# Kernel optimization log

Hardware: AMD Instinct MI355X
Metric: run time of the kernel (lower is better)

## Reference

```python
import jax, jax.numpy as jnp
import numpy as np

N = 100000   # nodes
E = 1600000  # edges (avg degree 16)
D = 128      # embedding / hidden dim
L = 2        # aggregator layers (len(weight_size_list)-1)
EPS = 1e-12  # F.normalize eps


def setup_inputs() -> dict:
    key = jax.random.key(0)
    ks = jax.random.split(key, 8)
    return {
        "embeddings": jax.random.normal(ks[0], (N, D), jnp.float32),
        "edge_src": jax.random.randint(ks[1], (E,), 0, N, jnp.int32),
        "edge_dst": jax.random.randint(ks[2], (E,), 0, N, jnp.int32),
        "edge_val": jax.random.uniform(ks[3], (E,), jnp.float32),
        "W_sum": jax.random.normal(ks[4], (L, D, D), jnp.float32) * 0.05,
        "b_sum": jnp.zeros((L, D), jnp.float32),
        "W_prod": jax.random.normal(ks[5], (L, D, D), jnp.float32) * 0.05,
        "b_prod": jnp.zeros((L, D), jnp.float32),
    }


def reference(embeddings, edge_src, edge_dst, edge_val, W_sum, b_sum, W_prod, b_prod):
    # Faithful KGATConv forward with BiAggregator (alg_type='bi'), dropout=0 (eval).
    # Note: original code feeds the UN-normalized aggregator output as `embeddings`
    # (ego) to the next layer, while the SpMM consumes the normalized all_embeddings[-1].
    ego = embeddings            # `embeddings` variable in torch code
    spmm_in = embeddings        # all_embeddings[-1]
    outs = [embeddings]
    for i in range(L):
        # sparse A @ x : gather source rows, scale by edge value, scatter-add to dst
        msg = edge_val[:, None] * spmm_in[edge_src]            # [E, D]
        side = jax.ops.segment_sum(msg, edge_dst, num_segments=N)  # [N, D]
        # BiAggregator: LeakyReLU(W1(e+side)+b1) + LeakyReLU(W2(e*side)+b2)
        s = jax.nn.leaky_relu((ego + side) @ W_sum[i] + b_sum[i], 0.01)
        p = jax.nn.leaky_relu((ego * side) @ W_prod[i] + b_prod[i], 0.01)
        ego = s + p
        # F.normalize(p=2, dim=-1)
        nrm = jnp.maximum(jnp.linalg.norm(ego, axis=-1, keepdims=True), EPS)
        spmm_in = ego / nrm
        outs.append(spmm_in)
    return jnp.stack(outs)  # [L+1, N, D]
```

## Files before the change

kernel.cpp:

```cpp
#include <hip/hip_runtime.h>

#define D_DIM 128
#define ROWS 32
#define MROWS 64
#define ZPAD 136
#define EPAD 132

#define BSH 7
#define BROWS (1 << BSH)
#define NB_MAX 2048
#define CHUNK 4096

typedef __bf16 bf16x8 __attribute__((ext_vector_type(8)));
typedef __bf16 bf16x4 __attribute__((ext_vector_type(4)));
typedef float  f32x4  __attribute__((ext_vector_type(4)));

__global__ __launch_bounds__(256) void spmm_atomic(
    const float* __restrict__ x, const int* __restrict__ src,
    const int* __restrict__ dst, const float* __restrict__ val,
    float* __restrict__ side, long long total)
{
    long long i = (long long)blockIdx.x * blockDim.x + threadIdx.x;
    if (i >= total) return;
    int e = (int)(i >> 5);
    int q = (int)(i & 31);
    int s = src[e];
    int d = dst[e];
    float v = val[e];
    const float4 xv = *reinterpret_cast<const float4*>(x + (long long)s * D_DIM + q * 4);
    float* o = side + (long long)d * D_DIM + q * 4;
    unsafeAtomicAdd(o + 0, v * xv.x);
    unsafeAtomicAdd(o + 1, v * xv.y);
    unsafeAtomicAdd(o + 2, v * xv.z);
    unsafeAtomicAdd(o + 3, v * xv.w);
}

__global__ __launch_bounds__(256) void hist_kernel(
    const int* __restrict__ dst, int* __restrict__ cnt, int E)
{
    int i = blockIdx.x * 256 + threadIdx.x;
    if (i < E) atomicAdd(&cnt[dst[i]], 1);
}

__global__ __launch_bounds__(256) void scan_blocks(
    const int* __restrict__ cnt, int* __restrict__ row_ptr,
    int* __restrict__ blk_sums, int N)
{
    __shared__ int sh[256];
    int i = blockIdx.x * 256 + threadIdx.x;
    int v = (i < N) ? cnt[i] : 0;
    sh[threadIdx.x] = v;
    __syncthreads();
#pragma unroll
    for (int off = 1; off < 256; off <<= 1) {
        int t = (threadIdx.x >= off) ? sh[threadIdx.x - off] : 0;
        __syncthreads();
        sh[threadIdx.x] += t;
        __syncthreads();
    }
    if (i < N) row_ptr[i] = sh[threadIdx.x] - v;
    if (threadIdx.x == 255) blk_sums[blockIdx.x] = sh[255];
}

__global__ __launch_bounds__(256) void scan_carry(int* __restrict__ blk, int B)
{
    __shared__ int sh[256];
    __shared__ int carry;
    if (threadIdx.x == 0) carry = 0;
    __syncthreads();
    for (int base = 0; base < B; base += 256) {
        int i = base + threadIdx.x;
        int v = (i < B) ? blk[i] : 0;
        sh[threadIdx.x] = v;
        __syncthreads();
#pragma unroll
        for (int off = 1; off < 256; off <<= 1) {
            int t = (threadIdx.x >= off) ? sh[threadIdx.x - off] : 0;
            __syncthreads();
            sh[threadIdx.x] += t;
            __syncthreads();
        }
        int excl = sh[threadIdx.x] - v + carry;
        if (i < B) blk[i] = excl;
        __syncthreads();
        if (threadIdx.x == 255) carry = carry + sh[255];
        __syncthreads();
    }
}

__global__ __launch_bounds__(256) void scan_add(
    int* __restrict__ row_ptr, const int* __restrict__ blk_sums,
    int* __restrict__ row_fill, int N, int E)
{
    int i = blockIdx.x * 256 + threadIdx.x;
    if (i < N) {
        int v = row_ptr[i] + blk_sums[i >> 8];
        row_ptr[i]  = v;
        row_fill[i] = v;
    }
    if (i == 0) row_ptr[N] = E;
}

__global__ __launch_bounds__(256) void scatter_kernel(
    const int* __restrict__ src, const int* __restrict__ dst,
    const float* __restrict__ val, int* __restrict__ row_fill,
    int2* __restrict__ csr_sv, int E)
{
    int e = blockIdx.x * 256 + threadIdx.x;
    if (e >= E) return;
    int d = dst[e];
    int pos = atomicAdd(&row_fill[d], 1);
    csr_sv[pos] = make_int2(src[e], __float_as_int(val[e]));
}

__global__ __launch_bounds__(256) void bucket_count(
    const int* __restrict__ dst, int* __restrict__ bucket_cnt, int E, int NB)
{
    __shared__ int h[NB_MAX];
    for (int i = threadIdx.x; i < NB; i += 256) h[i] = 0;
    __syncthreads();
    int ebase = blockIdx.x * CHUNK;
    int ecnt  = min(CHUNK, E - ebase);
    for (int i = threadIdx.x; i < ecnt; i += 256)
        atomicAdd(&h[dst[ebase + i] >> BSH], 1);
    __syncthreads();
    for (int i = threadIdx.x; i < NB; i += 256)
        if (h[i]) atomicAdd(&bucket_cnt[i], h[i]);
}

__global__ __launch_bounds__(256) void bucket_scan(
    const int* __restrict__ bucket_cnt, int* __restrict__ bucket_ptr,
    int* __restrict__ bucket_fill, int NB, int E)
{
    __shared__ int sh[256];
    __shared__ int carry;
    if (threadIdx.x == 0) carry = 0;
    __syncthreads();
    for (int base = 0; base < NB; base += 256) {
        int i = base + threadIdx.x;
        int v = (i < NB) ? bucket_cnt[i] : 0;
        sh[threadIdx.x] = v;
        __syncthreads();
#pragma unroll
        for (int off = 1; off < 256; off <<= 1) {
            int t = (threadIdx.x >= off) ? sh[threadIdx.x - off] : 0;
            __syncthreads();
            sh[threadIdx.x] += t;
            __syncthreads();
        }
        if (i < NB) {
            int excl = sh[threadIdx.x] - v + carry;
            bucket_ptr[i]  = excl;
            bucket_fill[i] = excl;
        }
        __syncthreads();
        if (threadIdx.x == 255) carry = carry + sh[255];
        __syncthreads();
    }
    if (threadIdx.x == 0) bucket_ptr[NB] = E;
}

__global__ __launch_bounds__(256) void bucket_scatter(
    const int* __restrict__ src, const int* __restrict__ dst,
    const float* __restrict__ val, int* __restrict__ bucket_fill,
    int* __restrict__ stage,
    int NB, int E)
{
    __shared__ int hist[NB_MAX];
    __shared__ int excl[NB_MAX];
    __shared__ int gbase[NB_MAX];
    __shared__ int psum[256];
    __shared__ int s_src[CHUNK];
    __shared__ int s_val[CHUNK];
    __shared__ int s_dst[CHUNK];

    const int tid   = threadIdx.x;
    const int ebase = blockIdx.x * CHUNK;
    const int ecnt  = min(CHUNK, E - ebase);

    for (int i = tid; i < NB; i += 256) hist[i] = 0;
    __syncthreads();
    for (int i = tid; i < ecnt; i += 256)
        atomicAdd(&hist[dst[ebase + i] >> BSH], 1);
    __syncthreads();
    const int per = (NB + 255) / 256;
    const int t0  = tid * per;
    int tsum = 0;
    for (int k = 0; k < per; ++k) {
        int idx = t0 + k;
        tsum += (idx < NB) ? hist[idx] : 0;
    }
    psum[tid] = tsum;
    __syncthreads();
#pragma unroll
    for (int off = 1; off < 256; off <<= 1) {
        int t = (tid >= off) ? psum[tid - off] : 0;
        __syncthreads();
        psum[tid] += t;
        __syncthreads();
    }
    int run = psum[tid] - tsum;
    for (int k = 0; k < per; ++k) {
        int idx = t0 + k;
        if (idx < NB) { excl[idx] = run; run += hist[idx]; }
    }
    __syncthreads();
    for (int i = tid; i < NB; i += 256)
        gbase[i] = hist[i] ? atomicAdd(&bucket_fill[i], hist[i]) : 0;
    __syncthreads();
    for (int i = tid; i < NB; i += 256) hist[i] = excl[i];
    __syncthreads();
    for (int i = tid; i < ecnt; i += 256) {
        int d = dst[ebase + i];
        int slot = atomicAdd(&hist[d >> BSH], 1);
        s_src[slot] = src[ebase + i];
        s_val[slot] = __float_as_int(val[ebase + i]);
        s_dst[slot] = d;
    }
    __syncthreads();
    for (int i = tid; i < ecnt; i += 256) {
        int d   = s_dst[i];
        int bkt = d >> BSH;
        int gpos = gbase[bkt] + (i - excl[bkt]);
        *reinterpret_cast<int4*>(stage + 4 * (long long)gpos) =
            make_int4(s_src[i], s_val[i], d, 0);
    }
}

__global__ __launch_bounds__(256) void bucket_finalize(
    const int* __restrict__ stage, const int* __restrict__ bucket_ptr,
    int* __restrict__ row_ptr, int2* __restrict__ csr_sv, int N, int E)
{
    __shared__ int cnt[BROWS];
    __shared__ int rbase[BROWS];

    const int b   = blockIdx.x;
    const int tid = threadIdx.x;
    const int e0  = bucket_ptr[b];
    const int e1  = bucket_ptr[b + 1];
    const int r0  = b << BSH;
    const int nrows = min(BROWS, N - r0);

    if (tid < BROWS) cnt[tid] = 0;
    __syncthreads();
    for (int i = e0 + tid; i < e1; i += 256)
        atomicAdd(&cnt[stage[4 * (long long)i + 2] & (BROWS - 1)], 1);
    __syncthreads();
    if (tid < BROWS) rbase[tid] = cnt[tid];
    __syncthreads();
#pragma unroll
    for (int off = 1; off < BROWS; off <<= 1) {
        int t = 0;
        if (tid < BROWS && tid >= off) t = rbase[tid - off];
        __syncthreads();
        if (tid < BROWS) rbase[tid] += t;
        __syncthreads();
    }
    if (tid < BROWS) {
        int excl = e0 + rbase[tid] - cnt[tid];
        rbase[tid] = excl;
        if (tid < nrows) row_ptr[r0 + tid] = excl;
    }
    if (b == 0 && tid == 0) row_ptr[N] = E;
    __syncthreads();
    if (tid < BROWS) cnt[tid] = 0;
    __syncthreads();
    for (int i = e0 + tid; i < e1; i += 256) {
        const int4 t = *reinterpret_cast<const int4*>(stage + 4 * (long long)i);
        int r = t.z & (BROWS - 1);
        int rank = atomicAdd(&cnt[r], 1);
        csr_sv[rbase[r] + rank] = make_int2(t.x, t.y);
    }
}

__global__ __launch_bounds__(256) void wt_convert(
    const float* __restrict__ Wsum, const float* __restrict__ Wprod,
    __bf16* __restrict__ WTsum, __bf16* __restrict__ WTprod, int total)
{
    int i = blockIdx.x * 256 + threadIdx.x;
    if (i >= total) return;
    int l  = i >> 14;
    int nk = i & 16383;
    int n  = nk >> 7;
    int k  = nk & 127;
    int widx = (l << 14) + (k << 7) + n;
    WTsum[i]  = (__bf16)Wsum[widx];
    WTprod[i] = (__bf16)Wprod[widx];
}

__global__ __launch_bounds__(256) void emb_prep(
    const float* __restrict__ emb, float* __restrict__ out0,
    __bf16* __restrict__ xbf, long long n4)
{
    long long i = (long long)blockIdx.x * 256 + threadIdx.x;
    if (i >= n4) return;
    float4 v = reinterpret_cast<const float4*>(emb)[i];
    reinterpret_cast<float4*>(out0)[i] = v;
    bf16x4 b;
    b[0] = (__bf16)v.x; b[1] = (__bf16)v.y;
    b[2] = (__bf16)v.z; b[3] = (__bf16)v.w;
    reinterpret_cast<bf16x4*>(xbf)[i] = b;
}

__global__ __launch_bounds__(256) void spmm_csr_bf16(
    const __bf16* __restrict__ x, const int* __restrict__ row_ptr,
    const int2* __restrict__ csr_sv, float* __restrict__ side, int N)
{
    int row  = blockIdx.x * 8 + (threadIdx.x >> 5);
    int lane = threadIdx.x & 31;
    if (row >= N) return;
    int start = row_ptr[row];
    int end   = row_ptr[row + 1];
    const __bf16* xl = x + lane * 4;
    float4 acc = make_float4(0.f, 0.f, 0.f, 0.f);
    int j = start;
    for (; j + 8 <= end; j += 8) {
        int2 sv0 = csr_sv[j + 0], sv1 = csr_sv[j + 1];
        int2 sv2 = csr_sv[j + 2], sv3 = csr_sv[j + 3];
        int2 sv4 = csr_sv[j + 4], sv5 = csr_sv[j + 5];
        int2 sv6 = csr_sv[j + 6], sv7 = csr_sv[j + 7];
        bf16x4 b0 = *reinterpret_cast<const bf16x4*>(xl + (long long)sv0.x * D_DIM);
        bf16x4 b1 = *reinterpret_cast<const bf16x4*>(xl + (long long)sv1.x * D_DIM);
        bf16x4 b2 = *reinterpret_cast<const bf16x4*>(xl + (long long)sv2.x * D_DIM);
        bf16x4 b3 = *reinterpret_cast<const bf16x4*>(xl + (long long)sv3.x * D_DIM);
        bf16x4 b4 = *reinterpret_cast<const bf16x4*>(xl + (long long)sv4.x * D_DIM);
        bf16x4 b5 = *reinterpret_cast<const bf16x4*>(xl + (long long)sv5.x * D_DIM);
        bf16x4 b6 = *reinterpret_cast<const bf16x4*>(xl + (long long)sv6.x * D_DIM);
        bf16x4 b7 = *reinterpret_cast<const bf16x4*>(xl + (long long)sv7.x * D_DIM);
        float v0 = __int_as_float(sv0.y), v1 = __int_as_float(sv1.y);
        float v2 = __int_as_float(sv2.y), v3 = __int_as_float(sv3.y);
        float v4 = __int_as_float(sv4.y), v5 = __int_as_float(sv5.y);
        float v6 = __int_as_float(sv6.y), v7 = __int_as_float(sv7.y);
        acc.x += v0 * (float)b0[0] + v1 * (float)b1[0] + v2 * (float)b2[0] + v3 * (float)b3[0];
        acc.y += v0 * (float)b0[1] + v1 * (float)b1[1] + v2 * (float)b2[1] + v3 * (float)b3[1];
        acc.z += v0 * (float)b0[2] + v1 * (float)b1[2] + v2 * (float)b2[2] + v3 * (float)b3[2];
        acc.w += v0 * (float)b0[3] + v1 * (float)b1[3] + v2 * (float)b2[3] + v3 * (float)b3[3];
        acc.x += v4 * (float)b4[0] + v5 * (float)b5[0] + v6 * (float)b6[0] + v7 * (float)b7[0];
        acc.y += v4 * (float)b4[1] + v5 * (float)b5[1] + v6 * (float)b6[1] + v7 * (float)b7[1];
        acc.z += v4 * (float)b4[2] + v5 * (float)b5[2] + v6 * (float)b6[2] + v7 * (float)b7[2];
        acc.w += v4 * (float)b4[3] + v5 * (float)b5[3] + v6 * (float)b6[3] + v7 * (float)b7[3];
    }
    for (; j + 4 <= end; j += 4) {
        int2 sv0 = csr_sv[j + 0], sv1 = csr_sv[j + 1];
        int2 sv2 = csr_sv[j + 2], sv3 = csr_sv[j + 3];
        bf16x4 b0 = *reinterpret_cast<const bf16x4*>(xl + (long long)sv0.x * D_DIM);
        bf16x4 b1 = *reinterpret_cast<const bf16x4*>(xl + (long long)sv1.x * D_DIM);
        bf16x4 b2 = *reinterpret_cast<const bf16x4*>(xl + (long long)sv2.x * D_DIM);
        bf16x4 b3 = *reinterpret_cast<const bf16x4*>(xl + (long long)sv3.x * D_DIM);
        float v0 = __int_as_float(sv0.y), v1 = __int_as_float(sv1.y);
        float v2 = __int_as_float(sv2.y), v3 = __int_as_float(sv3.y);
        acc.x += v0 * (float)b0[0] + v1 * (float)b1[0] + v2 * (float)b2[0] + v3 * (float)b3[0];
        acc.y += v0 * (float)b0[1] + v1 * (float)b1[1] + v2 * (float)b2[1] + v3 * (float)b3[1];
        acc.z += v0 * (float)b0[2] + v1 * (float)b1[2] + v2 * (float)b2[2] + v3 * (float)b3[2];
        acc.w += v0 * (float)b0[3] + v1 * (float)b1[3] + v2 * (float)b2[3] + v3 * (float)b3[3];
    }
    for (; j < end; ++j) {
        int2 sv = csr_sv[j];
        float v = __int_as_float(sv.y);
        bf16x4 b = *reinterpret_cast<const bf16x4*>(xl + (long long)sv.x * D_DIM);
        acc.x += v * (float)b[0];
        acc.y += v * (float)b[1];
        acc.z += v * (float)b[2];
        acc.w += v * (float)b[3];
    }
    *reinterpret_cast<float4*>(side + (long long)row * D_DIM + lane * 4) = acc;
}

__global__ __launch_bounds__(256) void spmm_csr_f32(
    const float* __restrict__ x, const int* __restrict__ row_ptr,
    const int2* __restrict__ csr_sv, float* __restrict__ side, int N)
{
    int row  = blockIdx.x * 8 + (threadIdx.x >> 5);
    int lane = threadIdx.x & 31;
    if (row >= N) return;
    int start = row_ptr[row];
    int end   = row_ptr[row + 1];
    const float* xl = x + lane * 4;
    float4 acc = make_float4(0.f, 0.f, 0.f, 0.f);
    int j = start;
    for (; j + 4 <= end; j += 4) {
        int2 sv0 = csr_sv[j + 0], sv1 = csr_sv[j + 1];
        int2 sv2 = csr_sv[j + 2], sv3 = csr_sv[j + 3];
        const float4 x0 = *reinterpret_cast<const float4*>(xl + (long long)sv0.x * D_DIM);
        const float4 x1 = *reinterpret_cast<const float4*>(xl + (long long)sv1.x * D_DIM);
        const float4 x2 = *reinterpret_cast<const float4*>(xl + (long long)sv2.x * D_DIM);
        const float4 x3 = *reinterpret_cast<const float4*>(xl + (long long)sv3.x * D_DIM);
        float v0 = __int_as_float(sv0.y), v1 = __int_as_float(sv1.y);
        float v2 = __int_as_float(sv2.y), v3 = __int_as_float(sv3.y);
        acc.x += v0 * x0.x + v1 * x1.x + v2 * x2.x + v3 * x3.x;
        acc.y += v0 * x0.y + v1 * x1.y + v2 * x2.y + v3 * x3.y;
        acc.z += v0 * x0.z + v1 * x1.z + v2 * x2.z + v3 * x3.z;
        acc.w += v0 * x0.w + v1 * x1.w + v2 * x2.w + v3 * x3.w;
    }
    for (; j < end; ++j) {
        int2 sv = csr_sv[j];
        float v = __int_as_float(sv.y);
        const float4 xv = *reinterpret_cast<const float4*>(xl + (long long)sv.x * D_DIM);
        acc.x += v * xv.x;
        acc.y += v * xv.y;
        acc.z += v * xv.z;
        acc.w += v * xv.w;
    }
    *reinterpret_cast<float4*>(side + (long long)row * D_DIM + lane * 4) = acc;
}

__global__ __launch_bounds__(512) void fused_layer_mfma(
    const float* __restrict__ ego_src, const float* __restrict__ nrm_in,
    const float* __restrict__ side,
    const __bf16* __restrict__ WTsum, const float* __restrict__ bsum,
    const __bf16* __restrict__ WTprod, const float* __restrict__ bprod,
    float* __restrict__ norm_out,
    __bf16* __restrict__ nbf_out,
    float* __restrict__ nrm_out,
    int N)
{
    __shared__ __align__(16) char smem[MROWS * ZPAD * 2 * sizeof(__bf16)];
    __shared__ float rowsq[MROWS][9];
    auto zt = reinterpret_cast<__bf16(*)[ZPAD]>(smem);
    auto mt = reinterpret_cast<__bf16(*)[ZPAD]>(smem + MROWS * ZPAD * sizeof(__bf16));
    auto et = reinterpret_cast<float(*)[EPAD]>(smem);

    const int tid  = threadIdx.x;
    const int row0 = blockIdx.x * MROWS;

    for (int idx = tid; idx < MROWS * 32; idx += 512) {
        int r = idx >> 5, q = idx & 31;
        int row = row0 + r;
        float4 e4 = make_float4(0.f, 0.f, 0.f, 0.f);
        float4 s4 = make_float4(0.f, 0.f, 0.f, 0.f);
        if (row < N) {
            e4 = *reinterpret_cast<const float4*>(ego_src + (long long)row * D_DIM + q * 4);
            s4 = *reinterpret_cast<const float4*>(side    + (long long)row * D_DIM + q * 4);
            if (nrm_in) {
                float sc = nrm_in[row];
                e4.x *= sc; e4.y *= sc; e4.z *= sc; e4.w *= sc;
            }
        }
        bf16x4 z4, m4;
        z4[0] = (__bf16)(e4.x + s4.x); z4[1] = (__bf16)(e4.y + s4.y);
        z4[2] = (__bf16)(e4.z + s4.z); z4[3] = (__bf16)(e4.w + s4.w);
        m4[0] = (__bf16)(e4.x * s4.x); m4[1] = (__bf16)(e4.y * s4.y);
        m4[2] = (__bf16)(e4.z * s4.z); m4[3] = (__bf16)(e4.w * s4.w);
        *reinterpret_cast<bf16x4*>(&zt[r][q * 4]) = z4;
        *reinterpret_cast<bf16x4*>(&mt[r][q * 4]) = m4;
    }

    const int wave = tid >> 6;
    const int lane = tid & 63;
    const int ln   = lane & 15;
    const int quad = lane >> 4;

    bf16x8 bs[4], bp[4];
#pragma unroll
    for (int ks = 0; ks < 4; ++ks) {
        const long long wofs = (long long)(wave * 16 + ln) * D_DIM + ks * 32 + quad * 8;
        bs[ks] = *reinterpret_cast<const bf16x8*>(WTsum  + wofs);
        bp[ks] = *reinterpret_cast<const bf16x8*>(WTprod + wofs);
    }

    __syncthreads();

    f32x4 acc_s[4], acc_p[4];
#pragma unroll
    for (int rg = 0; rg < 4; ++rg) {
        acc_s[rg] = (f32x4){0.f, 0.f, 0.f, 0.f};
        acc_p[rg] = (f32x4){0.f, 0.f, 0.f, 0.f};
    }

#pragma unroll
    for (int rg = 0; rg < 4; ++rg) {
#pragma unroll
        for (int ks = 0; ks < 4; ++ks) {
            const int k0 = ks * 32 + quad * 8;
            bf16x8 az = *reinterpret_cast<const bf16x8*>(&zt[rg * 16 + ln][k0]);
            bf16x8 am = *reinterpret_cast<const bf16x8*>(&mt[rg * 16 + ln][k0]);
            acc_s[rg] = __builtin_amdgcn_mfma_f32_16x16x32_bf16(az, bs[ks], acc_s[rg], 0, 0, 0);
            acc_p[rg] = __builtin_amdgcn_mfma_f32_16x16x32_bf16(am, bp[ks], acc_p[rg], 0, 0, 0);
        }
    }

    const float bsv = bsum[wave * 16 + ln];
    const float bpv = bprod[wave * 16 + ln];
#pragma unroll
    for (int rg = 0; rg < 4; ++rg) {
#pragma unroll
        for (int r = 0; r < 4; ++r) {
            float sv = acc_s[rg][r] + bsv;
            sv = sv > 0.f ? sv : 0.01f * sv;
            float pv = acc_p[rg][r] + bpv;
            pv = pv > 0.f ? pv : 0.01f * pv;
            float e = sv + pv;
            acc_s[rg][r] = e;
            float sq = e * e;
#pragma unroll
            for (int off = 1; off < 16; off <<= 1)
                sq += __shfl_xor(sq, off, 16);
            if (ln == 0)
                rowsq[rg * 16 + quad * 4 + r][wave] = sq;
        }
    }

    __syncthreads();

#pragma unroll
    for (int rg = 0; rg < 4; ++rg)
#pragma unroll
        for (int r = 0; r < 4; ++r)
            et[rg * 16 + quad * 4 + r][wave * 16 + ln] = acc_s[rg][r];
    __syncthreads();

    for (int idx = tid; idx < MROWS * 32; idx += 512) {
        int r = idx >> 5, q = idx & 31;
        int row = row0 + r;
        if (row >= N) continue;
        float s = 0.f;
#pragma unroll
        for (int j = 0; j < 8; ++j) s += rowsq[r][j];
        float nrmv = fmaxf(sqrtf(s), 1e-12f);
        float inv  = 1.0f / nrmv;
        if (q == 0 && nrm_out) nrm_out[row] = nrmv;
        float4 e4 = *reinterpret_cast<const float4*>(&et[r][q * 4]);
        float4 n4 = make_float4(e4.x * inv, e4.y * inv, e4.z * inv, e4.w * inv);
        *reinterpret_cast<float4*>(norm_out + (long long)row * D_DIM + q * 4) = n4;
        if (nbf_out) {
            bf16x4 b4;
            b4[0] = (__bf16)n4.x; b4[1] = (__bf16)n4.y;
            b4[2] = (__bf16)n4.z; b4[3] = (__bf16)n4.w;
            *reinterpret_cast<bf16x4*>(nbf_out + (long long)row * D_DIM + q * 4) = b4;
        }
    }
}

__global__ __launch_bounds__(256) void fused_layer_f32(
    const float* __restrict__ ego, const float* __restrict__ side,
    const float* __restrict__ Wsum, const float* __restrict__ bsum,
    const float* __restrict__ Wprod, const float* __restrict__ bprod,
    float* __restrict__ ego_out, float* __restrict__ norm_out, int N)
{
    __shared__ float zt[ROWS][D_DIM];
    __shared__ float mt[ROWS][D_DIM];
    __shared__ float wsh[32][D_DIM];
    __shared__ float wph[32][D_DIM];

    const int tid  = threadIdx.x;
    const int row0 = blockIdx.x * ROWS;
    const int cg   = tid & 31;
    const int rg   = tid >> 5;

    for (int idx = tid; idx < ROWS * 32; idx += 256) {
        int r = idx >> 5, q = idx & 31;
        int row = row0 + r;
        float4 e4 = make_float4(0.f, 0.f, 0.f, 0.f);
        float4 s4 = make_float4(0.f, 0.f, 0.f, 0.f);
        if (row < N) {
            e4 = *reinterpret_cast<const float4*>(ego  + (long long)row * D_DIM + q * 4);
            s4 = *reinterpret_cast<const float4*>(side + (long long)row * D_DIM + q * 4);
        }
        float4 z4 = make_float4(e4.x + s4.x, e4.y + s4.y, e4.z + s4.z, e4.w + s4.w);
        float4 m4 = make_float4(e4.x * s4.x, e4.y * s4.y, e4.z * s4.z, e4.w * s4.w);
        *reinterpret_cast<float4*>(&zt[r][q * 4]) = z4;
        *reinterpret_cast<float4*>(&mt[r][q * 4]) = m4;
    }

    float acc_s[4][4], acc_p[4][4];
#pragma unroll
    for (int a = 0; a < 4; ++a)
#pragma unroll
        for (int b = 0; b < 4; ++b) { acc_s[a][b] = 0.f; acc_p[a][b] = 0.f; }

    for (int kc = 0; kc < D_DIM; kc += 32) {
        __syncthreads();
        for (int idx = tid; idx < 32 * 32; idx += 256) {
            int kk = idx >> 5, q = idx & 31;
            *reinterpret_cast<float4*>(&wsh[kk][q * 4]) =
                *reinterpret_cast<const float4*>(Wsum + (long long)(kc + kk) * D_DIM + q * 4);
            *reinterpret_cast<float4*>(&wph[kk][q * 4]) =
                *reinterpret_cast<const float4*>(Wprod + (long long)(kc + kk) * D_DIM + q * 4);
        }
        __syncthreads();
#pragma unroll 8
        for (int kk = 0; kk < 32; ++kk) {
            float4 w_s = *reinterpret_cast<const float4*>(&wsh[kk][cg * 4]);
            float4 w_p = *reinterpret_cast<const float4*>(&wph[kk][cg * 4]);
#pragma unroll
            for (int rr = 0; rr < 4; ++rr) {
                float z = zt[rg * 4 + rr][kc + kk];
                float m = mt[rg * 4 + rr][kc + kk];
                acc_s[rr][0] += z * w_s.x; acc_s[rr][1] += z * w_s.y;
                acc_s[rr][2] += z * w_s.z; acc_s[rr][3] += z * w_s.w;
                acc_p[rr][0] += m * w_p.x; acc_p[rr][1] += m * w_p.y;
                acc_p[rr][2] += m * w_p.z; acc_p[rr][3] += m * w_p.w;
            }
        }
    }

    const float4 bs = *reinterpret_cast<const float4*>(bsum  + cg * 4);
    const float4 bp = *reinterpret_cast<const float4*>(bprod + cg * 4);
    float ev[4][4];
    float part[4];
#pragma unroll
    for (int rr = 0; rr < 4; ++rr) {
        float bsv[4] = {bs.x, bs.y, bs.z, bs.w};
        float bpv[4] = {bp.x, bp.y, bp.z, bp.w};
        float acc = 0.f;
#pragma unroll
        for (int cc = 0; cc < 4; ++cc) {
            float sv = acc_s[rr][cc] + bsv[cc];
            sv = sv > 0.f ? sv : 0.01f * sv;
            float pv = acc_p[rr][cc] + bpv[cc];
            pv = pv > 0.f ? pv : 0.01f * pv;
            float e = sv + pv;
            ev[rr][cc] = e;
            acc += e * e;
        }
        part[rr] = acc;
    }
#pragma unroll
    for (int off = 1; off < 32; off <<= 1) {
#pragma unroll
        for (int rr = 0; rr < 4; ++rr)
            part[rr] += __shfl_xor(part[rr], off, 32);
    }
#pragma unroll
    for (int rr = 0; rr < 4; ++rr) {
        int row = row0 + rg * 4 + rr;
        if (row >= N) continue;
        float inv = 1.0f / fmaxf(sqrtf(part[rr]), 1e-12f);
        float4 o  = make_float4(ev[rr][0] * inv, ev[rr][1] * inv,
                                ev[rr][2] * inv, ev[rr][3] * inv);
        *reinterpret_cast<float4*>(norm_out + (long long)row * D_DIM + cg * 4) = o;
        if (ego_out) {
            float4 g = make_float4(ev[rr][0], ev[rr][1], ev[rr][2], ev[rr][3]);
            *reinterpret_cast<float4*>(ego_out + (long long)row * D_DIM + cg * 4) = g;
        }
    }
}

extern "C" void kernel_launch(void* const* d_in, const int* in_sizes, int n_in,
                              void* d_out, int out_size, void* d_ws, size_t ws_size,
                              hipStream_t stream)
{
    const float* emb   = (const float*)d_in[0];
    const int*   esrc  = (const int*)  d_in[1];
    const int*   edst  = (const int*)  d_in[2];
    const float* evalv = (const float*)d_in[3];
    const float* Wsum  = (const float*)d_in[4];
    const float* bsum  = (const float*)d_in[5];
    const float* Wprod = (const float*)d_in[6];
    const float* bprod = (const float*)d_in[7];
    float* out = (float*)d_out;

    const int D = 128;
    const int N = in_sizes[0] / D;
    const int E = in_sizes[1];
    const int L = in_sizes[5] / D;
    const size_t ND = (size_t)N * D;
    const int B = (N + 255) / 256;
    const int NB = (N + BROWS - 1) >> BSH;

    char* ws = (char*)d_ws;
    float* side    = (float*)ws;                 ws += ND * sizeof(float);
    float* ego_buf = (float*)ws;                 ws += ND * sizeof(float);
    int*   row_ptr  = (int*)ws;                  ws += (size_t)(N + 1) * sizeof(int);
    int*   row_fill = (int*)ws;                  ws += (size_t)N * sizeof(int);
    int*   blk_sums = (int*)ws;                  ws += (size_t)B * sizeof(int);
    ws = (char*)(((uintptr_t)ws + 15) & ~(uintptr_t)15);
    int2*  csr_sv   = (int2*)ws;                 ws += (size_t)E * sizeof(int2);
    size_t csr_bytes = (size_t)(ws - (char*)d_ws);
    __bf16* WTsum  = (__bf16*)ws;                ws += (size_t)L * D * D * sizeof(__bf16);
    __bf16* WTprod = (__bf16*)ws;                ws += (size_t)L * D * D * sizeof(__bf16);
    __bf16* xbf    = (__bf16*)ws;                ws += ND * sizeof(__bf16);
    float*  nrm_buf = (float*)ws;                ws += (size_t)N * sizeof(float);
    size_t mfma_bytes = (size_t)(ws - (char*)d_ws);
    int* bucket_cnt  = (int*)ws;                 ws += (size_t)(NB + 1) * sizeof(int);
    int* bucket_ptr  = (int*)ws;                 ws += (size_t)(NB + 1) * sizeof(int);
    int* bucket_fill = (int*)ws;                 ws += (size_t)(NB + 1) * sizeof(int);
    size_t bucket_bytes = (size_t)(ws - (char*)d_ws);
    int* stage = (int*)side;

    const bool use_csr    = (ws_size >= csr_bytes);
    const bool use_mfma   = (ws_size >= mfma_bytes);
    const bool use_bucket = use_csr && (ws_size >= bucket_bytes) && (NB <= NB_MAX) &&
                            ((size_t)E * 16 <= 2 * ND * sizeof(float));

    if (use_mfma) {
        long long n4 = (long long)(ND / 4);
        emb_prep<<<(int)((n4 + 255) / 256), 256, 0, stream>>>(emb, out, xbf, n4);
        int total = L * D * D;
        wt_convert<<<(total + 255) / 256, 256, 0, stream>>>(
            Wsum, Wprod, WTsum, WTprod, total);
    } else {
        hipMemcpyAsync(out, emb, ND * sizeof(float), hipMemcpyDeviceToDevice, stream);
    }

    if (use_bucket) {
        const int nblk = (E + CHUNK - 1) / CHUNK;
        hipMemsetAsync(bucket_cnt, 0, (size_t)NB * sizeof(int), stream);
        bucket_count<<<nblk, 256, 0, stream>>>(edst, bucket_cnt, E, NB);
        bucket_scan<<<1, 256, 0, stream>>>(bucket_cnt, bucket_ptr, bucket_fill, NB, E);
        bucket_scatter<<<nblk, 256, 0, stream>>>(
            esrc, edst, evalv, bucket_fill, stage, NB, E);
        bucket_finalize<<<NB, 256, 0, stream>>>(
            stage, bucket_ptr, row_ptr, csr_sv, N, E);
    } else if (use_csr) {
        hipMemsetAsync(row_fill, 0, (size_t)N * sizeof(int), stream);
        hist_kernel<<<(E + 255) / 256, 256, 0, stream>>>(edst, row_fill, E);
        scan_blocks<<<B, 256, 0, stream>>>(row_fill, row_ptr, blk_sums, N);
        scan_carry<<<1, 256, 0, stream>>>(blk_sums, B);
        scan_add<<<B, 256, 0, stream>>>(row_ptr, blk_sums, row_fill, N, E);
        scatter_kernel<<<(E + 255) / 256, 256, 0, stream>>>(
            esrc, edst, evalv, row_fill, csr_sv, E);
    }

    const float* ego      = emb;
    const float* nrm_prev = nullptr;
    const float* spmm_in  = emb;
    for (int l = 0; l < L; ++l) {
        if (use_csr) {
            if (use_mfma) {
                spmm_csr_bf16<<<(N + 7) / 8, 256, 0, stream>>>(
                    xbf, row_ptr, csr_sv, side, N);
            } else {
                spmm_csr_f32<<<(N + 7) / 8, 256, 0, stream>>>(
                    spmm_in, row_ptr, csr_sv, side, N);
            }
        } else {
            hipMemsetAsync(side, 0, ND * sizeof(float), stream);
            long long total  = (long long)E * 32;
            long long blocks = (total + 255) / 256;
            spmm_atomic<<<(int)blocks, 256, 0, stream>>>(spmm_in, esrc, edst, evalv,
                                                         side, total);
        }

        float* norm_out = out + (size_t)(l + 1) * ND;
        if (use_mfma) {
            const bool more = (l + 1 < L);
            __bf16* nbf  = more ? xbf : nullptr;
            float*  nrmo = more ? nrm_buf : nullptr;
            fused_layer_mfma<<<(N + MROWS - 1) / MROWS, 512, 0, stream>>>(
                ego, nrm_prev, side,
                WTsum + (size_t)l * D * D, bsum + (size_t)l * D,
                WTprod + (size_t)l * D * D, bprod + (size_t)l * D,
                norm_out, nbf, nrmo, N);
            ego      = norm_out;
            nrm_prev = nrm_buf;
        } else {
            float* ego_out = (l + 1 < L) ? ego_buf : nullptr;
            fused_layer_f32<<<(N + ROWS - 1) / ROWS, 256, 0, stream>>>(
                ego, side,
                Wsum + (size_t)l * D * D, bsum + (size_t)l * D,
                Wprod + (size_t)l * D * D, bprod + (size_t)l * D,
                ego_out, norm_out, N);
            ego     = ego_buf;
            spmm_in = norm_out;
        }
    }
}
```

Measured before the change: 535.0 us.

## Pack bucket staging into int2, fuse prep kernels, use nontemporal stores

The bucket staging record shrinks from int4 to int2 by packing the row-within-bucket index into the high bits of the source index, which halves staging traffic. NB_MAX drops from 2048 to 1024, cutting shared memory in bucket_scatter. The embedding-prep and weight-transpose kernels become one launch, and the out0 and SpMM side writes use nontemporal stores. The packing limits N to 2^17, now checked in the host condition, and NB=782 still fits under the new NB_MAX.

```diff
diff --git a/kernel.cpp b/kernel.cpp
--- a/kernel.cpp
+++ b/kernel.cpp
@@ -8,7 +8,7 @@
 
 #define BSH 7
 #define BROWS (1 << BSH)
-#define NB_MAX 2048
+#define NB_MAX 1024
 #define CHUNK 4096
 
 typedef __bf16 bf16x8 __attribute__((ext_vector_type(8)));
@@ -163,7 +163,7 @@
 __global__ __launch_bounds__(256) void bucket_scatter(
     const int* __restrict__ src, const int* __restrict__ dst,
     const float* __restrict__ val, int* __restrict__ bucket_fill,
-    int* __restrict__ stage,
+    int2* __restrict__ stage,
     int NB, int E)
 {
     __shared__ int hist[NB_MAX];
@@ -222,13 +222,12 @@
         int d   = s_dst[i];
         int bkt = d >> BSH;
         int gpos = gbase[bkt] + (i - excl[bkt]);
-        *reinterpret_cast<int4*>(stage + 4 * (long long)gpos) =
-            make_int4(s_src[i], s_val[i], d, 0);
+        stage[gpos] = make_int2(s_src[i] | ((d & (BROWS - 1)) << 17), s_val[i]);
     }
 }
 
 __global__ __launch_bounds__(256) void bucket_finalize(
-    const int* __restrict__ stage, const int* __restrict__ bucket_ptr,
+    const int2* __restrict__ stage, const int* __restrict__ bucket_ptr,
     int* __restrict__ row_ptr, int2* __restrict__ csr_sv, int N, int E)
 {
     __shared__ int cnt[BROWS];
@@ -244,7 +243,7 @@
     if (tid < BROWS) cnt[tid] = 0;
     __syncthreads();
     for (int i = e0 + tid; i < e1; i += 256)
-        atomicAdd(&cnt[stage[4 * (long long)i + 2] & (BROWS - 1)], 1);
+        atomicAdd(&cnt[(stage[i].x >> 17) & (BROWS - 1)], 1);
     __syncthreads();
     if (tid < BROWS) rbase[tid] = cnt[tid];
     __syncthreads();
@@ -266,40 +265,40 @@
     if (tid < BROWS) cnt[tid] = 0;
     __syncthreads();
     for (int i = e0 + tid; i < e1; i += 256) {
-        const int4 t = *reinterpret_cast<const int4*>(stage + 4 * (long long)i);
-        int r = t.z & (BROWS - 1);
+        const int2 t = stage[i];
+        int r = (t.x >> 17) & (BROWS - 1);
         int rank = atomicAdd(&cnt[r], 1);
-        csr_sv[rbase[r] + rank] = make_int2(t.x, t.y);
-    }
-}
-
-__global__ __launch_bounds__(256) void wt_convert(
+        csr_sv[rbase[r] + rank] = make_int2(t.x & 0x1FFFF, t.y);
+    }
+}
+
+__global__ __launch_bounds__(256) void prep_kernel(
+    const float* __restrict__ emb, float* __restrict__ out0,
+    __bf16* __restrict__ xbf, long long n4,
     const float* __restrict__ Wsum, const float* __restrict__ Wprod,
-    __bf16* __restrict__ WTsum, __bf16* __restrict__ WTprod, int total)
-{
-    int i = blockIdx.x * 256 + threadIdx.x;
-    if (i >= total) return;
-    int l  = i >> 14;
-    int nk = i & 16383;
-    int n  = nk >> 7;
-    int k  = nk & 127;
-    int widx = (l << 14) + (k << 7) + n;
-    WTsum[i]  = (__bf16)Wsum[widx];
-    WTprod[i] = (__bf16)Wprod[widx];
-}
-
-__global__ __launch_bounds__(256) void emb_prep(
-    const float* __restrict__ emb, float* __restrict__ out0,
-    __bf16* __restrict__ xbf, long long n4)
+    __bf16* __restrict__ WTsum, __bf16* __restrict__ WTprod, int wtotal)
 {
     long long i = (long long)blockIdx.x * 256 + threadIdx.x;
-    if (i >= n4) return;
-    float4 v = reinterpret_cast<const float4*>(emb)[i];
-    reinterpret_cast<float4*>(out0)[i] = v;
-    bf16x4 b;
-    b[0] = (__bf16)v.x; b[1] = (__bf16)v.y;
-    b[2] = (__bf16)v.z; b[3] = (__bf16)v.w;
-    reinterpret_cast<bf16x4*>(xbf)[i] = b;
+    if (i < n4) {
+        float4 v = reinterpret_cast<const float4*>(emb)[i];
+        f32x4 nv = {v.x, v.y, v.z, v.w};
+        __builtin_nontemporal_store(nv, reinterpret_cast<f32x4*>(out0) + i);
+        bf16x4 b;
+        b[0] = (__bf16)v.x; b[1] = (__bf16)v.y;
+        b[2] = (__bf16)v.z; b[3] = (__bf16)v.w;
+        reinterpret_cast<bf16x4*>(xbf)[i] = b;
+    } else {
+        int k = (int)(i - n4);
+        if (k < wtotal) {
+            int l  = k >> 14;
+            int nk = k & 16383;
+            int n  = nk >> 7;
+            int kk = nk & 127;
+            int widx = (l << 14) + (kk << 7) + n;
+            WTsum[k]  = (__bf16)Wsum[widx];
+            WTprod[k] = (__bf16)Wprod[widx];
+        }
+    }
 }
 
 __global__ __launch_bounds__(256) void spmm_csr_bf16(
@@ -363,7 +362,9 @@
         acc.z += v * (float)b[2];
         acc.w += v * (float)b[3];
     }
-    *reinterpret_cast<float4*>(side + (long long)row * D_DIM + lane * 4) = acc;
+    f32x4 nv = {acc.x, acc.y, acc.z, acc.w};
+    __builtin_nontemporal_store(
+        nv, reinterpret_cast<f32x4*>(side + (long long)row * D_DIM + lane * 4));
 }
 
 __global__ __launch_bounds__(256) void spmm_csr_f32(
@@ -676,19 +677,20 @@
     int* bucket_ptr  = (int*)ws;                 ws += (size_t)(NB + 1) * sizeof(int);
     int* bucket_fill = (int*)ws;                 ws += (size_t)(NB + 1) * sizeof(int);
     size_t bucket_bytes = (size_t)(ws - (char*)d_ws);
-    int* stage = (int*)side;
+    int2* stage = (int2*)side;
 
     const bool use_csr    = (ws_size >= csr_bytes);
     const bool use_mfma   = (ws_size >= mfma_bytes);
     const bool use_bucket = use_csr && (ws_size >= bucket_bytes) && (NB <= NB_MAX) &&
-                            ((size_t)E * 16 <= 2 * ND * sizeof(float));
+                            (N <= (1 << 17)) &&
+                            ((size_t)E * sizeof(int2) <= ND * sizeof(float));
 
     if (use_mfma) {
         long long n4 = (long long)(ND / 4);
-        emb_prep<<<(int)((n4 + 255) / 256), 256, 0, stream>>>(emb, out, xbf, n4);
-        int total = L * D * D;
-        wt_convert<<<(total + 255) / 256, 256, 0, stream>>>(
-            Wsum, Wprod, WTsum, WTprod, total);
+        int wtotal = L * D * D;
+        long long total = n4 + wtotal;
+        prep_kernel<<<(int)((total + 255) / 256), 256, 0, stream>>>(
+            emb, out, xbf, n4, Wsum, Wprod, WTsum, WTprod, wtotal);
     } else {
         hipMemcpyAsync(out, emb, ND * sizeof(float), hipMemcpyDeviceToDevice, stream);
     }
```

New measurement: 562.6 us. 1.05x slower.
